# Kernel optimization log

Measured on AMD Instinct MI355X. Metric: run time of the kernel, lower is better.

The kernel has to match this reference:

```python
import jax, jax.numpy as jnp
import numpy as np

NODE_NUM = 8192   # 's' nodes
SEQ_LEN = 192     # 't' nodes
N = NODE_NUM + SEQ_LEN
C = 128
B = 2
E = 262144


def setup_inputs() -> dict:
    key = jax.random.key(0)
    ks = jax.random.split(key, 6)
    x = jax.random.normal(ks[0], (B, N, C), dtype=jnp.float32)
    edge_index = jax.random.randint(ks[1], (B, 2, E), 0, N)
    s = 1.0 / np.sqrt(2 * C)  # Linear default init range
    W_ss = jax.random.uniform(ks[2], (2, 2 * C), jnp.float32, -s, s)
    W_tt = jax.random.uniform(ks[3], (2, 2 * C), jnp.float32, -s, s)
    W_st = jax.random.uniform(ks[4], (2, 2 * C), jnp.float32, -s, s)
    W_ts = jax.random.uniform(ks[5], (2, 2 * C), jnp.float32, -s, s)
    return {"x": x, "edge_index": edge_index, "W_ss": W_ss, "W_tt": W_tt,
            "W_st": W_st, "W_ts": W_ts}


def _edge_alpha(xi, xj, W):
    # att_g(concat([x_i, x_j])).tanh(); W is [2C], concat order is [x_i, x_j]
    return jnp.tanh(xi @ W[:C] + xj @ W[C:])


def _intra(x, src, dst, W_ss, W_tt):
    # SSConv on s-s edges + TTConv on t-t edges, gcn_norm with self loops
    m_ss = (src < NODE_NUM) & (dst < NODE_NUM)
    m_tt = (src >= NODE_NUM) & (dst >= NODE_NUM)
    w = (m_ss | m_tt).astype(x.dtype)
    # degrees per homogeneous subgraph (targets are disjoint) + self loop
    deg = jax.ops.segment_sum(w, dst, num_segments=N) + 1.0
    dinv = deg ** -0.5
    xi = x[dst]            # [E, C]
    xj = x[src]            # [E, C]
    alpha = jnp.where(m_ss, _edge_alpha(xi, xj, W_ss), _edge_alpha(xi, xj, W_tt))
    coef = alpha * w * dinv[src] * dinv[dst]            # [E]
    out = jax.ops.segment_sum(xj * coef[:, None], dst, num_segments=N)
    # self-loop messages: x_i = x_j = x, norm = 1/deg
    is_s = jnp.arange(N) < NODE_NUM
    a_self = jnp.where(is_s, _edge_alpha(x, x, W_ss), _edge_alpha(x, x, W_tt))
    out = out + x * (a_self / deg)[:, None]
    return x + out


def _inter(x, src, dst, W_st, W_ts):
    # STConv on s->t edges + TSConv on t->s edges, directed in-degree norm
    m_st = (src < NODE_NUM) & (dst >= NODE_NUM)
    m_ts = (src >= NODE_NUM) & (dst < NODE_NUM)
    w = (m_st | m_ts).astype(x.dtype)
    deg = jax.ops.segment_sum(w, dst, num_segments=N)
    dinv = jnp.where(deg > 0, 1.0 / jnp.where(deg > 0, deg, 1.0), 0.0)
    xi = x[dst]
    xj = x[src]
    alpha = jnp.where(m_st, _edge_alpha(xi, xj, W_st), _edge_alpha(xi, xj, W_ts))
    coef = alpha * w * dinv[dst]
    out = jax.ops.segment_sum(xj * coef[:, None], dst, num_segments=N)
    return x + out


def reference(x, edge_index, W_ss, W_tt, W_st, W_ts):
    # n_layers = 4: intra, inter, intra, inter; relu after every layer but last
    def one_graph(xb, eb):
        src, dst = eb[0], eb[1]
        h = xb
        for li in range(2):
            h = jax.nn.relu(_intra(h, src, dst, W_ss[li], W_tt[li]))
            h = _inter(h, src, dst, W_st[li], W_ts[li])
            if li < 1:
                h = jax.nn.relu(h)
        return h
    return jax.vmap(one_graph)(x, edge_index)
```

## Files before the change

kernel.cpp:

```cpp
#include <hip/hip_runtime.h>
#include <stdint.h>

#define NODE_NUM 8192
#define NN 8384
#define CC 128
#define BB 2
#define EE 262144
#define CAP 128
#define CAP2 120
#define P_B 131
#define CAPP 4096
#define FILLB 256

__device__ __forceinline__ unsigned int f2bf_u(float f) {
  unsigned int u = __float_as_uint(f);
  return (u + 0x7FFFu + ((u >> 16) & 1u)) >> 16;
}
__device__ __forceinline__ float bf2f(unsigned int u) {
  return __uint_as_float(u << 16);
}

__global__ void k_part_init(const int* __restrict__ ei,
                            int* __restrict__ partCur, unsigned int* __restrict__ partBuf,
                            const float* __restrict__ x, unsigned int* __restrict__ xb,
                            const float* __restrict__ Wi_s, const float* __restrict__ Wj_s,
                            const float* __restrict__ Wi_t, const float* __restrict__ Wj_t,
                            float* __restrict__ pi, float2* __restrict__ pjn) {
  if (blockIdx.x < FILLB) {
    __shared__ unsigned int sEdge[2048];
    __shared__ int sCnt[P_B];
    __shared__ int sOff[P_B + 1];
    __shared__ int sBase[P_B];
    int tid = threadIdx.x;
    int b = blockIdx.x >> 7;
    int e0 = (blockIdx.x & 127) * 2048;
    const int* eb = ei + b * 2 * EE;
    for (int i = tid; i < P_B; i += 256) sCnt[i] = 0;
    __syncthreads();
    const int4* s4 = (const int4*)(eb + e0 + tid * 8);
    const int4* d4 = (const int4*)(eb + EE + e0 + tid * 8);
    int4 sa = s4[0], sb_ = s4[1], da = d4[0], db_ = d4[1];
    int srcs[8] = {sa.x, sa.y, sa.z, sa.w, sb_.x, sb_.y, sb_.z, sb_.w};
    int dsts[8] = {da.x, da.y, da.z, da.w, db_.x, db_.y, db_.z, db_.w};
    unsigned int cache[8];
#pragma unroll
    for (int k = 0; k < 8; ++k) {
      int src = srcs[k], dst = dsts[k];
      if ((unsigned)src >= NN || (unsigned)dst >= NN) { cache[k] = 0xFFFFFFFFu; continue; }
      int p = dst >> 6;
      cache[k] = ((unsigned)p << 20) | ((unsigned)(dst & 63) << 14) | (unsigned)src;
      atomicAdd(&sCnt[p], 1);
    }
    __syncthreads();
    if (tid == 0) {
      int acc = 0;
      for (int i = 0; i < P_B; ++i) { sOff[i] = acc; acc += sCnt[i]; }
      sOff[P_B] = acc;
    }
    __syncthreads();
    if (tid < P_B) sBase[tid] = atomicAdd(&partCur[b * P_B + tid], sCnt[tid]);
    __syncthreads();
    if (tid < P_B) sCnt[tid] = 0;
    __syncthreads();
#pragma unroll
    for (int k = 0; k < 8; ++k) {
      unsigned int v = cache[k];
      if (v == 0xFFFFFFFFu) continue;
      int p = v >> 20;
      int pos = atomicAdd(&sCnt[p], 1);
      sEdge[sOff[p] + pos] = v;
    }
    __syncthreads();
    int total = sOff[P_B];
    for (int i = tid; i < total; i += 256) {
      unsigned int v = sEdge[i];
      int p = v >> 20;
      int idx = (i - sOff[p]) + sBase[p];
      if (idx < CAPP)
        partBuf[(size_t)(b * P_B + p) * CAPP + idx] = v & 0xFFFFFu;
    }
  } else {
    int wid = ((blockIdx.x - FILLB) * blockDim.x + threadIdx.x) >> 6;
    int lane = threadIdx.x & 63;
    int n = wid % NN;
    bool is_s = (n < NODE_NUM);
    const float* wi = is_s ? Wi_s : Wi_t;
    const float* wj = is_s ? Wj_s : Wj_t;
    size_t oi = (size_t)wid * (CC / 2) + lane;
    float2 hv = ((const float2*)x)[oi];
    xb[oi] = (f2bf_u(hv.y) << 16) | f2bf_u(hv.x);
    float2 wiv = *(const float2*)(wi + lane * 2);
    float2 wjv = *(const float2*)(wj + lane * 2);
    float a = hv.x * wiv.x + hv.y * wiv.y;
    float c = hv.x * wjv.x + hv.y * wjv.y;
#pragma unroll
    for (int o = 32; o > 0; o >>= 1) {
      a += __shfl_xor(a, o, 64);
      c += __shfl_xor(c, o, 64);
    }
    if (lane == 0) { pi[wid] = a; pjn[wid].x = c; }
  }
}

__global__ void k_bucket(const int* __restrict__ partCur, const unsigned int* __restrict__ partBuf,
                         int* __restrict__ cur_intra, int* __restrict__ cur_inter,
                         int* __restrict__ colS_intra, int* __restrict__ colS_inter,
                         float* __restrict__ dinv_intra, float* __restrict__ selfnorm,
                         float* __restrict__ dinv_inter, float2* __restrict__ pjn0) {
  __shared__ unsigned int sIn[32 * CAP2];
  __shared__ unsigned int sIt[32 * CAP2];
  __shared__ int sC[64];
  int tid = threadIdx.x;
  int task = blockIdx.x;
  int gp = task >> 1;
  int half = task & 1;
  int b = gp / P_B;
  int p = gp - b * P_B;
  if (tid < 64) sC[tid] = 0;
  __syncthreads();
  int cnt = partCur[gp];
  cnt = cnt < CAPP ? cnt : CAPP;
  const unsigned int* buf = partBuf + (size_t)gp * CAPP;
  for (int i = tid; i < cnt; i += 256) {
    unsigned int v = buf[i];
    int off = (v >> 14) & 63;
    if ((off >> 5) != half) continue;
    int o = off & 31;
    int src = v & 0x3FFF;
    int dst = p * 64 + off;
    bool ss = (src < NODE_NUM) && (dst < NODE_NUM);
    bool tt = (src >= NODE_NUM) && (dst >= NODE_NUM);
    if (ss || tt) {
      int pos = atomicAdd(&sC[o], 1);
      if (pos < CAP2) sIn[o * CAP2 + pos] = src;
    } else {
      int pos = atomicAdd(&sC[32 + o], 1);
      if (pos < CAP2) sIt[o * CAP2 + pos] = src;
    }
  }
  __syncthreads();
  int dbase = p * 64 + half * 32;
  size_t gbase = ((size_t)b * NN + dbase) * CAP;
  for (int j = tid; j < 32 * CAP; j += 256) {
    int off = j >> 7, slot = j & (CAP - 1);
    int ci = sC[off];      ci = ci < CAP2 ? ci : CAP2;
    int ct = sC[32 + off]; ct = ct < CAP2 ? ct : CAP2;
    if (slot < ci) colS_intra[gbase + j] = (int)sIn[off * CAP2 + slot];
    if (slot < ct) colS_inter[gbase + j] = (int)sIt[off * CAP2 + slot];
  }
  if (tid < 32) {
    int node = b * NN + dbase + tid;
    int ci = sC[tid];       ci = ci < CAP2 ? ci : CAP2;
    int ct = sC[32 + tid];  ct = ct < CAP2 ? ct : CAP2;
    cur_intra[node] = ci;
    cur_inter[node] = ct;
    float df = (float)(ci + 1);
    float di = rsqrtf(df);
    dinv_intra[node] = di;
    selfnorm[node] = 1.0f / df;
    dinv_inter[node] = (ct > 0) ? (1.0f / (float)ct) : 0.0f;
    pjn0[node].y = di;
  }
}

template <bool INTRA, bool RELU, bool NEXTPROJ, bool NEXT_INTRA>
__global__ void __launch_bounds__(256, 6)
k_gather(const float* __restrict__ h_in, const unsigned int* __restrict__ hm,
         float* __restrict__ h_out, unsigned int* __restrict__ hm_out,
         const int* __restrict__ cnt, const int* __restrict__ colS,
         const float* __restrict__ pi, const float2* __restrict__ pjn,
         const float* __restrict__ normD, const float* __restrict__ selfnorm,
         const float* __restrict__ dinv_intra,
         const float* __restrict__ nWi_s, const float* __restrict__ nWj_s,
         const float* __restrict__ nWi_t, const float* __restrict__ nWj_t,
         float* __restrict__ pi_out, float2* __restrict__ pjn_out) {
  int wid = (blockIdx.x * blockDim.x + threadIdx.x) >> 6;
  int lane = threadIdx.x & 63;
  int b = wid / NN;
  int n = wid - b * NN;
  int mt = cnt[wid];
  mt = mt < CAP ? mt : CAP;
  const float* hb = h_in + (size_t)b * NN * CC;
  const unsigned int* hmb = hm + (size_t)b * NN * (CC / 2) + lane;
  const float2* pjnb = pjn + b * NN;
  float p_i = pi[wid];
  float nd = normD[wid];
  const float2 hv = *(const float2*)(hb + (size_t)n * CC + lane * 2);
  float2 acc;
  if (INTRA) {
    float fac = 1.0f + tanhf(p_i + pjnb[n].x) * selfnorm[wid];
    acc.x = hv.x * fac;
    acc.y = hv.y * fac;
  } else {
    acc = hv;
  }
  const int* cS = colS + (size_t)wid * CAP;
  for (int off = 0; off < mt; off += 64) {
    int rem = mt - off;
    int m = rem < 64 ? rem : 64;
    int src = 0;
    float c = 0.0f;
    if (lane < m) {
      src = cS[off + lane];
      float2 pn = pjnb[src];
      float a = tanhf(p_i + pn.x);
      c = a * nd;
      if (INTRA) c *= pn.y;
    }
#pragma unroll
    for (int base = 0; base < 64; base += 16) {
      if (base >= m) break;
      unsigned int u[16];
      float cj[16];
#pragma unroll
      for (int k = 0; k < 16; ++k) {
        int sj = __builtin_amdgcn_readlane(src, base + k);
        cj[k] = __int_as_float(
            __builtin_amdgcn_readlane(__float_as_int(c), base + k));
        u[k] = hmb[sj * (CC / 2)];
      }
#pragma unroll
      for (int k = 0; k < 16; ++k) {
        acc.x = fmaf(bf2f(u[k] & 0xFFFFu), cj[k], acc.x);
        acc.y = fmaf(bf2f(u[k] >> 16), cj[k], acc.y);
      }
    }
  }
  if (RELU) { acc.x = fmaxf(acc.x, 0.0f); acc.y = fmaxf(acc.y, 0.0f); }
  size_t oi = (size_t)wid * (CC / 2) + lane;
  *(float2*)(h_out + 2 * oi) = acc;
  if (NEXTPROJ) {
    hm_out[oi] = (f2bf_u(acc.y) << 16) | f2bf_u(acc.x);
    bool is_s = (n < NODE_NUM);
    const float* wi = is_s ? nWi_s : nWi_t;
    const float* wj = is_s ? nWj_s : nWj_t;
    float2 wiv = *(const float2*)(wi + lane * 2);
    float2 wjv = *(const float2*)(wj + lane * 2);
    float a = acc.x * wiv.x + acc.y * wiv.y;
    float c2 = acc.x * wjv.x + acc.y * wjv.y;
#pragma unroll
    for (int o = 32; o > 0; o >>= 1) {
      a += __shfl_xor(a, o, 64);
      c2 += __shfl_xor(c2, o, 64);
    }
    if (lane == 0) {
      pi_out[wid] = a;
      float2 pn;
      pn.x = c2;
      pn.y = NEXT_INTRA ? dinv_intra[wid] : 0.0f;
      pjn_out[wid] = pn;
    }
  }
}

extern "C" void kernel_launch(void* const* d_in, const int* in_sizes, int n_in,
                              void* d_out, int out_size, void* d_ws, size_t ws_size,
                              hipStream_t stream) {
  const float* x = (const float*)d_in[0];
  const int* ei = (const int*)d_in[1];
  const float* Wss = (const float*)d_in[2];
  const float* Wtt = (const float*)d_in[3];
  const float* Wst = (const float*)d_in[4];
  const float* Wts = (const float*)d_in[5];
  float* out = (float*)d_out;

  char* p = (char*)d_ws;
  auto alloc = [&](size_t bytes) {
    void* r = (void*)p;
    p += ((bytes + 255) & ~(size_t)255);
    return r;
  };
  float* h0 = (float*)alloc((size_t)BB * NN * CC * 4);
  float* h1 = (float*)alloc((size_t)BB * NN * CC * 4);
  unsigned int* xb = (unsigned int*)alloc((size_t)BB * NN * CC * 2);
  unsigned int* mb0 = (unsigned int*)alloc((size_t)BB * NN * CC * 2);
  unsigned int* mb1 = (unsigned int*)alloc((size_t)BB * NN * CC * 2);
  float* pi0 = (float*)alloc(BB * NN * 4);
  float* pi1 = (float*)alloc(BB * NN * 4);
  float2* pjn0 = (float2*)alloc(BB * NN * 8);
  float2* pjn1 = (float2*)alloc(BB * NN * 8);
  float* dinv_intra = (float*)alloc(BB * NN * 4);
  float* selfnorm = (float*)alloc(BB * NN * 4);
  float* dinv_inter = (float*)alloc(BB * NN * 4);
  int* cur_intra = (int*)alloc(BB * NN * 4);
  int* cur_inter = (int*)alloc(BB * NN * 4);
  int* colS_intra = (int*)alloc((size_t)BB * NN * CAP * 4);
  int* colS_inter = (int*)alloc((size_t)BB * NN * CAP * 4);
  int* partCur = (int*)alloc(BB * P_B * 4);
  unsigned int* partBuf = (unsigned int*)alloc((size_t)BB * P_B * CAPP * 4);

  hipMemsetAsync(partCur, 0, BB * P_B * 4, stream);

  const int NODE_BLOCKS = (BB * NN * 64) / 256;
  const float* wss0 = Wss, *wtt0 = Wtt, *wst0 = Wst, *wts0 = Wts;
  const float* wss1 = Wss + 256, *wtt1 = Wtt + 256, *wst1 = Wst + 256, *wts1 = Wts + 256;

  k_part_init<<<FILLB + NODE_BLOCKS, 256, 0, stream>>>(
      ei, partCur, partBuf, x, xb, wss0, wss0 + 128, wtt0, wtt0 + 128, pi0, pjn0);
  k_bucket<<<BB * P_B * 2, 256, 0, stream>>>(partCur, partBuf, cur_intra, cur_inter,
                                             colS_intra, colS_inter,
                                             dinv_intra, selfnorm, dinv_inter, pjn0);

  k_gather<true, true, true, false><<<NODE_BLOCKS, 256, 0, stream>>>(
      x, xb, h0, mb0, cur_intra, colS_intra, pi0, pjn0, dinv_intra, selfnorm, dinv_intra,
      wts0, wst0 + 128, wst0, wts0 + 128, pi1, pjn1);

  k_gather<false, true, true, true><<<NODE_BLOCKS, 256, 0, stream>>>(
      h0, mb0, h1, mb1, cur_inter, colS_inter, pi1, pjn1, dinv_inter, selfnorm, dinv_intra,
      wss1, wss1 + 128, wtt1, wtt1 + 128, pi0, pjn0);

  k_gather<true, true, true, false><<<NODE_BLOCKS, 256, 0, stream>>>(
      h1, mb1, h0, mb0, cur_intra, colS_intra, pi0, pjn0, dinv_intra, selfnorm, dinv_intra,
      wts1, wst1 + 128, wst1, wts1 + 128, pi1, pjn1);

  k_gather<false, false, false, false><<<NODE_BLOCKS, 256, 0, stream>>>(
      h0, mb0, out, nullptr, cur_inter, colS_inter, pi1, pjn1, dinv_inter, selfnorm,
      dinv_intra, nullptr, nullptr, nullptr, nullptr, nullptr, nullptr);
}
```

Baseline: 144.5 us.

## Pre-scale bf16 messages by dinv, use fixed-run partition buffers, process four nodes per wave

Edge partitioning now writes into fixed per-chunk runs with byte counts. This drops the global atomics, the prefix scan, the LDS staging and the memset, at the cost of capping each run at 48 edges. The bf16 copy of x (and of the intra-layer messages) is pre-multiplied by the source node's dinv. The gather therefore no longer loads a float2 pjn per neighbour and reads a plain float pj instead. The bf16 conversion moves into the bucket kernel. Each wave now loops over four nodes with a smaller grid, which amortises launch and setup cost but reduces parallelism.

```diff
diff --git a/kernel.cpp b/kernel.cpp
--- a/kernel.cpp
+++ b/kernel.cpp
@@ -9,8 +9,10 @@
 #define CAP 128
 #define CAP2 120
 #define P_B 131
-#define CAPP 4096
+#define NCHUNK 128
+#define RUNL 48
 #define FILLB 256
+#define GBLK 1048
 
 __device__ __forceinline__ unsigned int f2bf_u(float f) {
   unsigned int u = __float_as_uint(f);
@@ -20,20 +22,18 @@
   return __uint_as_float(u << 16);
 }
 
-__global__ void k_part_init(const int* __restrict__ ei,
-                            int* __restrict__ partCur, unsigned int* __restrict__ partBuf,
-                            const float* __restrict__ x, unsigned int* __restrict__ xb,
-                            const float* __restrict__ Wi_s, const float* __restrict__ Wj_s,
-                            const float* __restrict__ Wi_t, const float* __restrict__ Wj_t,
-                            float* __restrict__ pi, float2* __restrict__ pjn) {
+__global__ void k_init(const int* __restrict__ ei,
+                       unsigned int* __restrict__ partBuf, unsigned char* __restrict__ cnt8,
+                       const float* __restrict__ x,
+                       const float* __restrict__ Wi_s, const float* __restrict__ Wj_s,
+                       const float* __restrict__ Wi_t, const float* __restrict__ Wj_t,
+                       float* __restrict__ pi, float* __restrict__ pj) {
+  int tid = threadIdx.x;
   if (blockIdx.x < FILLB) {
-    __shared__ unsigned int sEdge[2048];
     __shared__ int sCnt[P_B];
-    __shared__ int sOff[P_B + 1];
-    __shared__ int sBase[P_B];
-    int tid = threadIdx.x;
     int b = blockIdx.x >> 7;
-    int e0 = (blockIdx.x & 127) * 2048;
+    int chunk = blockIdx.x & (NCHUNK - 1);
+    int e0 = chunk * 2048;
     const int* eb = ei + b * 2 * EE;
     for (int i = tid; i < P_B; i += 256) sCnt[i] = 0;
     __syncthreads();
@@ -42,87 +42,73 @@
     int4 sa = s4[0], sb_ = s4[1], da = d4[0], db_ = d4[1];
     int srcs[8] = {sa.x, sa.y, sa.z, sa.w, sb_.x, sb_.y, sb_.z, sb_.w};
     int dsts[8] = {da.x, da.y, da.z, da.w, db_.x, db_.y, db_.z, db_.w};
-    unsigned int cache[8];
 #pragma unroll
     for (int k = 0; k < 8; ++k) {
       int src = srcs[k], dst = dsts[k];
-      if ((unsigned)src >= NN || (unsigned)dst >= NN) { cache[k] = 0xFFFFFFFFu; continue; }
+      if ((unsigned)src >= NN || (unsigned)dst >= NN) continue;
       int p = dst >> 6;
-      cache[k] = ((unsigned)p << 20) | ((unsigned)(dst & 63) << 14) | (unsigned)src;
-      atomicAdd(&sCnt[p], 1);
+      int pos = atomicAdd(&sCnt[p], 1);
+      if (pos < RUNL)
+        partBuf[(size_t)((b * P_B + p) * NCHUNK + chunk) * RUNL + pos] =
+            ((unsigned)(dst & 63) << 14) | (unsigned)src;
     }
     __syncthreads();
-    if (tid == 0) {
-      int acc = 0;
-      for (int i = 0; i < P_B; ++i) { sOff[i] = acc; acc += sCnt[i]; }
-      sOff[P_B] = acc;
-    }
-    __syncthreads();
-    if (tid < P_B) sBase[tid] = atomicAdd(&partCur[b * P_B + tid], sCnt[tid]);
-    __syncthreads();
-    if (tid < P_B) sCnt[tid] = 0;
-    __syncthreads();
-#pragma unroll
-    for (int k = 0; k < 8; ++k) {
-      unsigned int v = cache[k];
-      if (v == 0xFFFFFFFFu) continue;
-      int p = v >> 20;
-      int pos = atomicAdd(&sCnt[p], 1);
-      sEdge[sOff[p] + pos] = v;
-    }
-    __syncthreads();
-    int total = sOff[P_B];
-    for (int i = tid; i < total; i += 256) {
-      unsigned int v = sEdge[i];
-      int p = v >> 20;
-      int idx = (i - sOff[p]) + sBase[p];
-      if (idx < CAPP)
-        partBuf[(size_t)(b * P_B + p) * CAPP + idx] = v & 0xFFFFFu;
+    if (tid < P_B) {
+      int c = sCnt[tid];
+      cnt8[(b * P_B + tid) * NCHUNK + chunk] = (unsigned char)(c < RUNL ? c : RUNL);
     }
   } else {
-    int wid = ((blockIdx.x - FILLB) * blockDim.x + threadIdx.x) >> 6;
-    int lane = threadIdx.x & 63;
-    int n = wid % NN;
-    bool is_s = (n < NODE_NUM);
-    const float* wi = is_s ? Wi_s : Wi_t;
-    const float* wj = is_s ? Wj_s : Wj_t;
-    size_t oi = (size_t)wid * (CC / 2) + lane;
-    float2 hv = ((const float2*)x)[oi];
-    xb[oi] = (f2bf_u(hv.y) << 16) | f2bf_u(hv.x);
-    float2 wiv = *(const float2*)(wi + lane * 2);
-    float2 wjv = *(const float2*)(wj + lane * 2);
-    float a = hv.x * wiv.x + hv.y * wiv.y;
-    float c = hv.x * wjv.x + hv.y * wjv.y;
-#pragma unroll
-    for (int o = 32; o > 0; o >>= 1) {
-      a += __shfl_xor(a, o, 64);
-      c += __shfl_xor(c, o, 64);
-    }
-    if (lane == 0) { pi[wid] = a; pjn[wid].x = c; }
-  }
-}
-
-__global__ void k_bucket(const int* __restrict__ partCur, const unsigned int* __restrict__ partBuf,
+    int gw = (blockIdx.x - FILLB) * 4 + (tid >> 6);
+    int lane = tid & 63;
+#pragma unroll 1
+    for (int t = 0; t < 4; ++t) {
+      int wid = gw * 4 + t;
+      int b = wid >= NN;
+      int n = wid - b * NN;
+      bool is_s = (n < NODE_NUM);
+      const float* wi = is_s ? Wi_s : Wi_t;
+      const float* wj = is_s ? Wj_s : Wj_t;
+      float2 hv = ((const float2*)x)[(size_t)wid * (CC / 2) + lane];
+      float2 wiv = *(const float2*)(wi + lane * 2);
+      float2 wjv = *(const float2*)(wj + lane * 2);
+      float a = hv.x * wiv.x + hv.y * wiv.y;
+      float c = hv.x * wjv.x + hv.y * wjv.y;
+#pragma unroll
+      for (int o = 32; o > 0; o >>= 1) {
+        a += __shfl_xor(a, o, 64);
+        c += __shfl_xor(c, o, 64);
+      }
+      if (lane == 0) { pi[wid] = a; pj[wid] = c; }
+    }
+  }
+}
+
+__global__ void k_bucket(const unsigned int* __restrict__ partBuf,
+                         const unsigned char* __restrict__ cnt8,
+                         const float* __restrict__ x, unsigned int* __restrict__ xbs,
                          int* __restrict__ cur_intra, int* __restrict__ cur_inter,
                          int* __restrict__ colS_intra, int* __restrict__ colS_inter,
                          float* __restrict__ dinv_intra, float* __restrict__ selfnorm,
-                         float* __restrict__ dinv_inter, float2* __restrict__ pjn0) {
+                         float* __restrict__ dinv_inter) {
   __shared__ unsigned int sIn[32 * CAP2];
   __shared__ unsigned int sIt[32 * CAP2];
   __shared__ int sC[64];
+  __shared__ unsigned char sN[NCHUNK];
+  __shared__ float sDin[32];
   int tid = threadIdx.x;
-  int task = blockIdx.x;
-  int gp = task >> 1;
-  int half = task & 1;
+  int gp = blockIdx.x >> 1;
+  int half = blockIdx.x & 1;
   int b = gp / P_B;
   int p = gp - b * P_B;
   if (tid < 64) sC[tid] = 0;
+  if (tid < NCHUNK) sN[tid] = cnt8[gp * NCHUNK + tid];
   __syncthreads();
-  int cnt = partCur[gp];
-  cnt = cnt < CAPP ? cnt : CAPP;
-  const unsigned int* buf = partBuf + (size_t)gp * CAPP;
-  for (int i = tid; i < cnt; i += 256) {
-    unsigned int v = buf[i];
+  const unsigned int* buf = partBuf + (size_t)gp * (NCHUNK * RUNL);
+  for (int s = tid; s < NCHUNK * RUNL; s += 256) {
+    unsigned c = (unsigned)s / RUNL;
+    unsigned k = (unsigned)s - c * RUNL;
+    if (k >= sN[c]) continue;
+    unsigned int v = buf[s];
     int off = (v >> 14) & 63;
     if ((off >> 5) != half) continue;
     int o = off & 31;
@@ -159,96 +145,100 @@
     dinv_intra[node] = di;
     selfnorm[node] = 1.0f / df;
     dinv_inter[node] = (ct > 0) ? (1.0f / (float)ct) : 0.0f;
-    pjn0[node].y = di;
-  }
-}
-
-template <bool INTRA, bool RELU, bool NEXTPROJ, bool NEXT_INTRA>
+    sDin[tid] = di;
+  }
+  __syncthreads();
+  for (int j = tid; j < 32 * (CC / 2); j += 256) {
+    int node = j >> 6, col = j & 63;
+    size_t gi = ((size_t)(b * NN + dbase + node)) * (CC / 2) + col;
+    float2 hv = ((const float2*)x)[gi];
+    float sc = sDin[node];
+    xbs[gi] = (f2bf_u(hv.y * sc) << 16) | f2bf_u(hv.x * sc);
+  }
+}
+
+template <bool INTRA, bool RELU, bool NEXTPROJ, bool SCALE_MB>
 __global__ void __launch_bounds__(256, 6)
 k_gather(const float* __restrict__ h_in, const unsigned int* __restrict__ hm,
          float* __restrict__ h_out, unsigned int* __restrict__ hm_out,
          const int* __restrict__ cnt, const int* __restrict__ colS,
-         const float* __restrict__ pi, const float2* __restrict__ pjn,
+         const float* __restrict__ pi, const float* __restrict__ pj,
          const float* __restrict__ normD, const float* __restrict__ selfnorm,
          const float* __restrict__ dinv_intra,
          const float* __restrict__ nWi_s, const float* __restrict__ nWj_s,
          const float* __restrict__ nWi_t, const float* __restrict__ nWj_t,
-         float* __restrict__ pi_out, float2* __restrict__ pjn_out) {
-  int wid = (blockIdx.x * blockDim.x + threadIdx.x) >> 6;
+         float* __restrict__ pi_out, float* __restrict__ pj_out) {
+  int gw = blockIdx.x * 4 + (threadIdx.x >> 6);
   int lane = threadIdx.x & 63;
-  int b = wid / NN;
-  int n = wid - b * NN;
-  int mt = cnt[wid];
-  mt = mt < CAP ? mt : CAP;
-  const float* hb = h_in + (size_t)b * NN * CC;
-  const unsigned int* hmb = hm + (size_t)b * NN * (CC / 2) + lane;
-  const float2* pjnb = pjn + b * NN;
-  float p_i = pi[wid];
-  float nd = normD[wid];
-  const float2 hv = *(const float2*)(hb + (size_t)n * CC + lane * 2);
-  float2 acc;
-  if (INTRA) {
-    float fac = 1.0f + tanhf(p_i + pjnb[n].x) * selfnorm[wid];
-    acc.x = hv.x * fac;
-    acc.y = hv.y * fac;
-  } else {
-    acc = hv;
-  }
-  const int* cS = colS + (size_t)wid * CAP;
-  for (int off = 0; off < mt; off += 64) {
-    int rem = mt - off;
-    int m = rem < 64 ? rem : 64;
-    int src = 0;
-    float c = 0.0f;
-    if (lane < m) {
-      src = cS[off + lane];
-      float2 pn = pjnb[src];
-      float a = tanhf(p_i + pn.x);
-      c = a * nd;
-      if (INTRA) c *= pn.y;
-    }
-#pragma unroll
-    for (int base = 0; base < 64; base += 16) {
-      if (base >= m) break;
-      unsigned int u[16];
-      float cj[16];
-#pragma unroll
-      for (int k = 0; k < 16; ++k) {
-        int sj = __builtin_amdgcn_readlane(src, base + k);
-        cj[k] = __int_as_float(
-            __builtin_amdgcn_readlane(__float_as_int(c), base + k));
-        u[k] = hmb[sj * (CC / 2)];
+#pragma unroll 1
+  for (int t = 0; t < 4; ++t) {
+    int wid = gw * 4 + t;
+    int b = wid >= NN;
+    int n = wid - b * NN;
+    int mt = cnt[wid];
+    mt = mt < CAP ? mt : CAP;
+    const unsigned int* hmb = hm + (size_t)b * NN * (CC / 2) + lane;
+    const float* pjb = pj + b * NN;
+    float p_i = pi[wid];
+    float nd = normD[wid];
+    const float2 hv = *(const float2*)(h_in + (size_t)wid * CC + lane * 2);
+    float2 acc;
+    if (INTRA) {
+      float fac = 1.0f + tanhf(p_i + pjb[n]) * selfnorm[wid];
+      acc.x = hv.x * fac;
+      acc.y = hv.y * fac;
+    } else {
+      acc = hv;
+    }
+    const int* cS = colS + (size_t)wid * CAP;
+    for (int off = 0; off < mt; off += 64) {
+      int rem = mt - off;
+      int m = rem < 64 ? rem : 64;
+      int src = 0;
+      float c = 0.0f;
+      if (lane < m) {
+        src = cS[off + lane];
+        float a = tanhf(p_i + pjb[src]);
+        c = a * nd;
       }
 #pragma unroll
-      for (int k = 0; k < 16; ++k) {
-        acc.x = fmaf(bf2f(u[k] & 0xFFFFu), cj[k], acc.x);
-        acc.y = fmaf(bf2f(u[k] >> 16), cj[k], acc.y);
+      for (int base = 0; base < 64; base += 16) {
+        if (base >= m) break;
+        unsigned int u16[16];
+        float cj[16];
+#pragma unroll
+        for (int k = 0; k < 16; ++k) {
+          int sj = __builtin_amdgcn_readlane(src, base + k);
+          cj[k] = __int_as_float(
+              __builtin_amdgcn_readlane(__float_as_int(c), base + k));
+          u16[k] = hmb[sj * (CC / 2)];
+        }
+#pragma unroll
+        for (int k = 0; k < 16; ++k) {
+          acc.x = fmaf(bf2f(u16[k] & 0xFFFFu), cj[k], acc.x);
+          acc.y = fmaf(bf2f(u16[k] >> 16), cj[k], acc.y);
+        }
       }
     }
-  }
-  if (RELU) { acc.x = fmaxf(acc.x, 0.0f); acc.y = fmaxf(acc.y, 0.0f); }
-  size_t oi = (size_t)wid * (CC / 2) + lane;
-  *(float2*)(h_out + 2 * oi) = acc;
-  if (NEXTPROJ) {
-    hm_out[oi] = (f2bf_u(acc.y) << 16) | f2bf_u(acc.x);
-    bool is_s = (n < NODE_NUM);
-    const float* wi = is_s ? nWi_s : nWi_t;
-    const float* wj = is_s ? nWj_s : nWj_t;
-    float2 wiv = *(const float2*)(wi + lane * 2);
-    float2 wjv = *(const float2*)(wj + lane * 2);
-    float a = acc.x * wiv.x + acc.y * wiv.y;
-    float c2 = acc.x * wjv.x + acc.y * wjv.y;
-#pragma unroll
-    for (int o = 32; o > 0; o >>= 1) {
-      a += __shfl_xor(a, o, 64);
-      c2 += __shfl_xor(c2, o, 64);
-    }
-    if (lane == 0) {
-      pi_out[wid] = a;
-      float2 pn;
-      pn.x = c2;
-      pn.y = NEXT_INTRA ? dinv_intra[wid] : 0.0f;
-      pjn_out[wid] = pn;
+    if (RELU) { acc.x = fmaxf(acc.x, 0.0f); acc.y = fmaxf(acc.y, 0.0f); }
+    size_t oi = (size_t)wid * (CC / 2) + lane;
+    *(float2*)(h_out + 2 * oi) = acc;
+    if (NEXTPROJ) {
+      float msc = SCALE_MB ? dinv_intra[wid] : 1.0f;
+      hm_out[oi] = (f2bf_u(acc.y * msc) << 16) | f2bf_u(acc.x * msc);
+      bool is_s = (n < NODE_NUM);
+      const float* wi = is_s ? nWi_s : nWi_t;
+      const float* wj = is_s ? nWj_s : nWj_t;
+      float2 wiv = *(const float2*)(wi + lane * 2);
+      float2 wjv = *(const float2*)(wj + lane * 2);
+      float a = acc.x * wiv.x + acc.y * wiv.y;
+      float c2 = acc.x * wjv.x + acc.y * wjv.y;
+#pragma unroll
+      for (int o = 32; o > 0; o >>= 1) {
+        a += __shfl_xor(a, o, 64);
+        c2 += __shfl_xor(c2, o, 64);
+      }
+      if (lane == 0) { pi_out[wid] = a; pj_out[wid] = c2; }
     }
   }
 }
@@ -272,13 +262,13 @@
   };
   float* h0 = (float*)alloc((size_t)BB * NN * CC * 4);
   float* h1 = (float*)alloc((size_t)BB * NN * CC * 4);
-  unsigned int* xb = (unsigned int*)alloc((size_t)BB * NN * CC * 2);
+  unsigned int* xbs = (unsigned int*)alloc((size_t)BB * NN * CC * 2);
   unsigned int* mb0 = (unsigned int*)alloc((size_t)BB * NN * CC * 2);
   unsigned int* mb1 = (unsigned int*)alloc((size_t)BB * NN * CC * 2);
   float* pi0 = (float*)alloc(BB * NN * 4);
   float* pi1 = (float*)alloc(BB * NN * 4);
-  float2* pjn0 = (float2*)alloc(BB * NN * 8);
-  float2* pjn1 = (float2*)alloc(BB * NN * 8);
+  float* pj0 = (float*)alloc(BB * NN * 4);
+  float* pj1 = (float*)alloc(BB * NN * 4);
   float* dinv_intra = (float*)alloc(BB * NN * 4);
   float* selfnorm = (float*)alloc(BB * NN * 4);
   float* dinv_inter = (float*)alloc(BB * NN * 4);
@@ -286,34 +276,32 @@
   int* cur_inter = (int*)alloc(BB * NN * 4);
   int* colS_intra = (int*)alloc((size_t)BB * NN * CAP * 4);
   int* colS_inter = (int*)alloc((size_t)BB * NN * CAP * 4);
-  int* partCur = (int*)alloc(BB * P_B * 4);
-  unsigned int* partBuf = (unsigned int*)alloc((size_t)BB * P_B * CAPP * 4);
-
-  hipMemsetAsync(partCur, 0, BB * P_B * 4, stream);
-
-  const int NODE_BLOCKS = (BB * NN * 64) / 256;
+  unsigned char* cnt8 = (unsigned char*)alloc(BB * P_B * NCHUNK);
+  unsigned int* partBuf = (unsigned int*)alloc((size_t)BB * P_B * NCHUNK * RUNL * 4);
+
   const float* wss0 = Wss, *wtt0 = Wtt, *wst0 = Wst, *wts0 = Wts;
   const float* wss1 = Wss + 256, *wtt1 = Wtt + 256, *wst1 = Wst + 256, *wts1 = Wts + 256;
 
-  k_part_init<<<FILLB + NODE_BLOCKS, 256, 0, stream>>>(
-      ei, partCur, partBuf, x, xb, wss0, wss0 + 128, wtt0, wtt0 + 128, pi0, pjn0);
-  k_bucket<<<BB * P_B * 2, 256, 0, stream>>>(partCur, partBuf, cur_intra, cur_inter,
+  k_init<<<FILLB + GBLK, 256, 0, stream>>>(
+      ei, partBuf, cnt8, x, wss0, wss0 + 128, wtt0, wtt0 + 128, pi0, pj0);
+  k_bucket<<<BB * P_B * 2, 256, 0, stream>>>(partBuf, cnt8, x, xbs,
+                                             cur_intra, cur_inter,
                                              colS_intra, colS_inter,
-                                             dinv_intra, selfnorm, dinv_inter, pjn0);
-
-  k_gather<true, true, true, false><<<NODE_BLOCKS, 256, 0, stream>>>(
-      x, xb, h0, mb0, cur_intra, colS_intra, pi0, pjn0, dinv_intra, selfnorm, dinv_intra,
-      wts0, wst0 + 128, wst0, wts0 + 128, pi1, pjn1);
-
-  k_gather<false, true, true, true><<<NODE_BLOCKS, 256, 0, stream>>>(
-      h0, mb0, h1, mb1, cur_inter, colS_inter, pi1, pjn1, dinv_inter, selfnorm, dinv_intra,
-      wss1, wss1 + 128, wtt1, wtt1 + 128, pi0, pjn0);
-
-  k_gather<true, true, true, false><<<NODE_BLOCKS, 256, 0, stream>>>(
-      h1, mb1, h0, mb0, cur_intra, colS_intra, pi0, pjn0, dinv_intra, selfnorm, dinv_intra,
-      wts1, wst1 + 128, wst1, wts1 + 128, pi1, pjn1);
-
-  k_gather<false, false, false, false><<<NODE_BLOCKS, 256, 0, stream>>>(
-      h0, mb0, out, nullptr, cur_inter, colS_inter, pi1, pjn1, dinv_inter, selfnorm,
+                                             dinv_intra, selfnorm, dinv_inter);
+
+  k_gather<true, true, true, false><<<GBLK, 256, 0, stream>>>(
+      x, xbs, h0, mb0, cur_intra, colS_intra, pi0, pj0, dinv_intra, selfnorm,
+      dinv_intra, wts0, wst0 + 128, wst0, wts0 + 128, pi1, pj1);
+
+  k_gather<false, true, true, true><<<GBLK, 256, 0, stream>>>(
+      h0, mb0, h1, mb1, cur_inter, colS_inter, pi1, pj1, dinv_inter, selfnorm,
+      dinv_intra, wss1, wss1 + 128, wtt1, wtt1 + 128, pi0, pj0);
+
+  k_gather<true, true, true, false><<<GBLK, 256, 0, stream>>>(
+      h1, mb1, h0, mb0, cur_intra, colS_intra, pi0, pj0, dinv_intra, selfnorm,
+      dinv_intra, wts1, wst1 + 128, wst1, wts1 + 128, pi1, pj1);
+
+  k_gather<false, false, false, false><<<GBLK, 256, 0, stream>>>(
+      h0, mb0, out, nullptr, cur_inter, colS_inter, pi1, pj1, dinv_inter, selfnorm,
       dinv_intra, nullptr, nullptr, nullptr, nullptr, nullptr, nullptr);
 }
```

Result: slower. 167.2 us (+15.7%).

## Replace atomic partition append with fixed per-chunk runs and use fast tanh

Applied to the files above, without the earlier changes.

Edge partitioning no longer reserves space in a global per-partition buffer through atomics. Each edge chunk now writes its run for each partition into a fixed slot of up to 48 entries and records a byte count, which removes the memset and the global atomics. The bucket kernel scans all chunk slots and skips entries beyond each chunk's count, so it reads more sparse slots than before. The change also swaps tanhf for an exp/reciprocal approximation and simplifies the batch index math in the gather kernel, trading a little precision for fewer instructions.

```diff
diff --git a/kernel.cpp b/kernel.cpp
--- a/kernel.cpp
+++ b/kernel.cpp
@@ -9,7 +9,8 @@
 #define CAP 128
 #define CAP2 120
 #define P_B 131
-#define CAPP 4096
+#define NCHUNK 128
+#define RUNL 48
 #define FILLB 256
 
 __device__ __forceinline__ unsigned int f2bf_u(float f) {
@@ -19,21 +20,25 @@
 __device__ __forceinline__ float bf2f(unsigned int u) {
   return __uint_as_float(u << 16);
 }
-
-__global__ void k_part_init(const int* __restrict__ ei,
-                            int* __restrict__ partCur, unsigned int* __restrict__ partBuf,
-                            const float* __restrict__ x, unsigned int* __restrict__ xb,
-                            const float* __restrict__ Wi_s, const float* __restrict__ Wj_s,
-                            const float* __restrict__ Wi_t, const float* __restrict__ Wj_t,
-                            float* __restrict__ pi, float2* __restrict__ pjn) {
+__device__ __forceinline__ float fast_tanh(float x) {
+  float t = __expf(2.0f * x);
+  return 1.0f - 2.0f * __builtin_amdgcn_rcpf(t + 1.0f);
+}
+
+__global__ void k_init(const int* __restrict__ ei,
+                       unsigned int* __restrict__ partBuf, unsigned char* __restrict__ cnt8,
+                       const float* __restrict__ x, unsigned int* __restrict__ xb,
+                       const float* __restrict__ Wi_s, const float* __restrict__ Wj_s,
+                       const float* __restrict__ Wi_t, const float* __restrict__ Wj_t,
+                       float* __restrict__ pi, float2* __restrict__ pjn) {
+  int tid = threadIdx.x;
   if (blockIdx.x < FILLB) {
     __shared__ unsigned int sEdge[2048];
     __shared__ int sCnt[P_B];
     __shared__ int sOff[P_B + 1];
-    __shared__ int sBase[P_B];
-    int tid = threadIdx.x;
     int b = blockIdx.x >> 7;
-    int e0 = (blockIdx.x & 127) * 2048;
+    int chunk = blockIdx.x & (NCHUNK - 1);
+    int e0 = chunk * 2048;
     const int* eb = ei + b * 2 * EE;
     for (int i = tid; i < P_B; i += 256) sCnt[i] = 0;
     __syncthreads();
@@ -58,8 +63,6 @@
       sOff[P_B] = acc;
     }
     __syncthreads();
-    if (tid < P_B) sBase[tid] = atomicAdd(&partCur[b * P_B + tid], sCnt[tid]);
-    __syncthreads();
     if (tid < P_B) sCnt[tid] = 0;
     __syncthreads();
 #pragma unroll
@@ -75,9 +78,14 @@
     for (int i = tid; i < total; i += 256) {
       unsigned int v = sEdge[i];
       int p = v >> 20;
-      int idx = (i - sOff[p]) + sBase[p];
-      if (idx < CAPP)
-        partBuf[(size_t)(b * P_B + p) * CAPP + idx] = v & 0xFFFFFu;
+      int idx = i - sOff[p];
+      if (idx < RUNL)
+        partBuf[(size_t)((b * P_B + p) * NCHUNK + chunk) * RUNL + idx] =
+            v & 0xFFFFFu;
+    }
+    if (tid < P_B) {
+      int c = sCnt[tid];
+      cnt8[(b * P_B + tid) * NCHUNK + chunk] = (unsigned char)(c < RUNL ? c : RUNL);
     }
   } else {
     int wid = ((blockIdx.x - FILLB) * blockDim.x + threadIdx.x) >> 6;
@@ -102,7 +110,8 @@
   }
 }
 
-__global__ void k_bucket(const int* __restrict__ partCur, const unsigned int* __restrict__ partBuf,
+__global__ void k_bucket(const unsigned int* __restrict__ partBuf,
+                         const unsigned char* __restrict__ cnt8,
                          int* __restrict__ cur_intra, int* __restrict__ cur_inter,
                          int* __restrict__ colS_intra, int* __restrict__ colS_inter,
                          float* __restrict__ dinv_intra, float* __restrict__ selfnorm,
@@ -110,19 +119,21 @@
   __shared__ unsigned int sIn[32 * CAP2];
   __shared__ unsigned int sIt[32 * CAP2];
   __shared__ int sC[64];
+  __shared__ unsigned char sN[NCHUNK];
   int tid = threadIdx.x;
-  int task = blockIdx.x;
-  int gp = task >> 1;
-  int half = task & 1;
+  int gp = blockIdx.x >> 1;
+  int half = blockIdx.x & 1;
   int b = gp / P_B;
   int p = gp - b * P_B;
   if (tid < 64) sC[tid] = 0;
+  if (tid < NCHUNK) sN[tid] = cnt8[gp * NCHUNK + tid];
   __syncthreads();
-  int cnt = partCur[gp];
-  cnt = cnt < CAPP ? cnt : CAPP;
-  const unsigned int* buf = partBuf + (size_t)gp * CAPP;
-  for (int i = tid; i < cnt; i += 256) {
-    unsigned int v = buf[i];
+  const unsigned int* buf = partBuf + (size_t)gp * (NCHUNK * RUNL);
+  for (int s = tid; s < NCHUNK * RUNL; s += 256) {
+    int c = s / RUNL;
+    int k = s - c * RUNL;
+    if (k >= (int)sN[c]) continue;
+    unsigned int v = buf[s];
     int off = (v >> 14) & 63;
     if ((off >> 5) != half) continue;
     int o = off & 31;
@@ -176,19 +187,18 @@
          float* __restrict__ pi_out, float2* __restrict__ pjn_out) {
   int wid = (blockIdx.x * blockDim.x + threadIdx.x) >> 6;
   int lane = threadIdx.x & 63;
-  int b = wid / NN;
+  int b = wid >= NN;
   int n = wid - b * NN;
   int mt = cnt[wid];
   mt = mt < CAP ? mt : CAP;
-  const float* hb = h_in + (size_t)b * NN * CC;
   const unsigned int* hmb = hm + (size_t)b * NN * (CC / 2) + lane;
   const float2* pjnb = pjn + b * NN;
   float p_i = pi[wid];
   float nd = normD[wid];
-  const float2 hv = *(const float2*)(hb + (size_t)n * CC + lane * 2);
+  const float2 hv = *(const float2*)(h_in + (size_t)wid * CC + lane * 2);
   float2 acc;
   if (INTRA) {
-    float fac = 1.0f + tanhf(p_i + pjnb[n].x) * selfnorm[wid];
+    float fac = 1.0f + fast_tanh(p_i + pjnb[n].x) * selfnorm[wid];
     acc.x = hv.x * fac;
     acc.y = hv.y * fac;
   } else {
@@ -203,26 +213,26 @@
     if (lane < m) {
       src = cS[off + lane];
       float2 pn = pjnb[src];
-      float a = tanhf(p_i + pn.x);
+      float a = fast_tanh(p_i + pn.x);
       c = a * nd;
       if (INTRA) c *= pn.y;
     }
 #pragma unroll
     for (int base = 0; base < 64; base += 16) {
       if (base >= m) break;
-      unsigned int u[16];
+      unsigned int u16[16];
       float cj[16];
 #pragma unroll
       for (int k = 0; k < 16; ++k) {
         int sj = __builtin_amdgcn_readlane(src, base + k);
         cj[k] = __int_as_float(
             __builtin_amdgcn_readlane(__float_as_int(c), base + k));
-        u[k] = hmb[sj * (CC / 2)];
+        u16[k] = hmb[sj * (CC / 2)];
       }
 #pragma unroll
       for (int k = 0; k < 16; ++k) {
-        acc.x = fmaf(bf2f(u[k] & 0xFFFFu), cj[k], acc.x);
-        acc.y = fmaf(bf2f(u[k] >> 16), cj[k], acc.y);
+        acc.x = fmaf(bf2f(u16[k] & 0xFFFFu), cj[k], acc.x);
+        acc.y = fmaf(bf2f(u16[k] >> 16), cj[k], acc.y);
       }
     }
   }
@@ -286,18 +296,16 @@
   int* cur_inter = (int*)alloc(BB * NN * 4);
   int* colS_intra = (int*)alloc((size_t)BB * NN * CAP * 4);
   int* colS_inter = (int*)alloc((size_t)BB * NN * CAP * 4);
-  int* partCur = (int*)alloc(BB * P_B * 4);
-  unsigned int* partBuf = (unsigned int*)alloc((size_t)BB * P_B * CAPP * 4);
-
-  hipMemsetAsync(partCur, 0, BB * P_B * 4, stream);
+  unsigned char* cnt8 = (unsigned char*)alloc(BB * P_B * NCHUNK);
+  unsigned int* partBuf = (unsigned int*)alloc((size_t)BB * P_B * NCHUNK * RUNL * 4);
 
   const int NODE_BLOCKS = (BB * NN * 64) / 256;
   const float* wss0 = Wss, *wtt0 = Wtt, *wst0 = Wst, *wts0 = Wts;
   const float* wss1 = Wss + 256, *wtt1 = Wtt + 256, *wst1 = Wst + 256, *wts1 = Wts + 256;
 
-  k_part_init<<<FILLB + NODE_BLOCKS, 256, 0, stream>>>(
-      ei, partCur, partBuf, x, xb, wss0, wss0 + 128, wtt0, wtt0 + 128, pi0, pjn0);
-  k_bucket<<<BB * P_B * 2, 256, 0, stream>>>(partCur, partBuf, cur_intra, cur_inter,
+  k_init<<<FILLB + NODE_BLOCKS, 256, 0, stream>>>(
+      ei, partBuf, cnt8, x, xb, wss0, wss0 + 128, wtt0, wtt0 + 128, pi0, pjn0);
+  k_bucket<<<BB * P_B * 2, 256, 0, stream>>>(partBuf, cnt8, cur_intra, cur_inter,
                                              colS_intra, colS_inter,
                                              dinv_intra, selfnorm, dinv_inter, pjn0);
 
```

Result: no change. 145.4 us (+0.6%).
